# Optimization experiments

Hardware: AMD Instinct MI355X
Metric: run time of the kernel (lower is better)

Reference implementation:

```python
import jax, jax.numpy as jnp
import numpy as np

TEMPERATURE = 0.04


def _d3tod2(t):
    # 'c h w -> (h w) c'
    c, h, w = t.shape
    return jnp.transpose(t, (1, 2, 0)).reshape(h * w, c)


def setup_inputs() -> dict:
    key = jax.random.key(0)
    k1, k2 = jax.random.split(key)
    B, C, H, W = 4, 128, 96, 96
    # scale 0.05 keeps dot/temperature in a numerically sane range for exp
    x = jax.random.normal(k1, (B, C, H, W), dtype=jnp.float32) * 0.05
    label = jax.random.randint(k2, (B, 1, H, W), 0, 3, dtype=jnp.int32)
    return {"x": x, "label": label}


def reference(x, label):
    B, C, H, W = x.shape
    hw = H * W
    feat_1 = _d3tod2(x[0])                     # [HW, C]
    feat_2 = _d3tod2(x[1])                     # [HW, C]
    gt1 = label[0, 0].reshape(hw)              # [HW]
    gt2 = label[1, 0].reshape(hw)              # [HW]
    sim = jnp.exp(jnp.matmul(feat_1, feat_2.T) / TEMPERATURE)  # [HW, HW]
    mask = gt1[:, None] == gt2[None, :]        # [HW, HW] label-equality
    pos_sum = jnp.sum(jnp.where(mask, sim, jnp.zeros((), sim.dtype)))
    total_sum = jnp.sum(sim)
    loss = -jnp.log(pos_sum / total_sum) / (hw * hw)
    return loss
```

## Files before the change

### kernel.cpp

```cpp
#include <hip/hip_runtime.h>
#include <hip/hip_bf16.h>

#define HW 9216
#define CDIM 128
#define BM 256
#define BN 64
#define JT 4
#define GRID_I (HW / BM)
#define GRID_J (HW / (BN * JT))
#define NPART (GRID_I * GRID_J)
#define LDP (CDIM + 8)
#define SCH (HW / 512)

using bf16 = __hip_bfloat16;
typedef __attribute__((ext_vector_type(16))) float f32x16;
typedef __attribute__((ext_vector_type(8))) short s16x8;

#define EXP_SCALE 36.067376022224085f

#if __has_builtin(__builtin_amdgcn_exp2f)
#define FEXP2(x) __builtin_amdgcn_exp2f(x)
#else
#define FEXP2(x) exp2f(x)
#endif

__global__ __launch_bounds__(512) void sort_kernel(const int* __restrict__ label,
                                                   int* __restrict__ perm,
                                                   int* __restrict__ labs) {
    const int side = blockIdx.x;
    const int* L = label + side * HW;
    int* P = perm + side * HW;
    int* S = labs + side * HW;
    __shared__ int cnt[3][512];

    int t = threadIdx.x;
    int l[SCH];
    int c0 = 0, c1 = 0, c2 = 0;
#pragma unroll
    for (int k = 0; k < SCH; ++k) {
        l[k] = L[t * SCH + k];
        c0 += (l[k] == 0); c1 += (l[k] == 1); c2 += (l[k] == 2);
    }
    cnt[0][t] = c0; cnt[1][t] = c1; cnt[2][t] = c2;
    __syncthreads();

    for (int off = 1; off < 512; off <<= 1) {
        int v0 = cnt[0][t], v1 = cnt[1][t], v2 = cnt[2][t];
        int a0 = 0, a1 = 0, a2 = 0;
        if (t >= off) { a0 = cnt[0][t - off]; a1 = cnt[1][t - off]; a2 = cnt[2][t - off]; }
        __syncthreads();
        cnt[0][t] = v0 + a0; cnt[1][t] = v1 + a1; cnt[2][t] = v2 + a2;
        __syncthreads();
    }

    int i0 = cnt[0][t], i1 = cnt[1][t], i2 = cnt[2][t];
    int tl0 = cnt[0][511], tl1 = cnt[1][511];
    int o0 = i0 - c0;
    int o1 = tl0 + i1 - c1;
    int o2 = tl0 + tl1 + i2 - c2;
#pragma unroll
    for (int k = 0; k < SCH; ++k) {
        int lab = l[k];
        int pos = (lab == 0) ? o0++ : ((lab == 1) ? o1++ : o2++);
        P[pos] = t * SCH + k;
        S[pos] = lab;
    }
}

__global__ __launch_bounds__(256) void prep_kernel(const float* __restrict__ x,
                                                   const int* __restrict__ perm,
                                                   bf16* __restrict__ feat) {
    __shared__ float tile[64][65];
    const float* xs = x + (size_t)blockIdx.z * CDIM * HW;
    const int* permS = perm + blockIdx.z * HW;
    bf16* fs = feat + (size_t)blockIdx.z * HW * CDIM;
    float scale = (blockIdx.z == 0) ? EXP_SCALE : 1.0f;

    int p0 = blockIdx.x * 64;
    int c0 = blockIdx.y * 64;
    int t  = threadIdx.x;

    int pc = t & 63;
    int cr = t >> 6;
    int pidx = permS[p0 + pc];
#pragma unroll
    for (int i = 0; i < 16; ++i) {
        int cl = cr + i * 4;
        tile[cl][pc] = xs[(size_t)(c0 + cl) * HW + pidx];
    }
    __syncthreads();

    int cc = t & 63;
    int pr = t >> 6;
#pragma unroll
    for (int i = 0; i < 16; ++i) {
        int pl = pr + i * 4;
        fs[(size_t)(p0 + pl) * CDIM + c0 + cc] = __float2bfloat16(tile[cc][pl] * scale);
    }
}

__global__ __launch_bounds__(512, 4) void simsum_kernel(const bf16* __restrict__ feat1,
                                                        const bf16* __restrict__ feat2,
                                                        const int* __restrict__ labs,
                                                        float* __restrict__ partials) {
    __shared__ bf16 Bs[2][BN][LDP];
    __shared__ float red[16];

    const int* lab1s = labs;
    const int* lab2s = labs + HW;

    int t    = threadIdx.x;
    int w    = t >> 6;
    int lane = t & 63;
    int cl   = lane & 31;
    int hi   = lane >> 5;

    int i0  = blockIdx.x * BM;
    int jb  = blockIdx.y * (BN * JT);
    int r0w = i0 + w * 32;

    s16x8 af[8];
    {
        const bf16* arow = &feat1[(size_t)(r0w + cl) * CDIM + hi * 8];
#pragma unroll
        for (int s = 0; s < 8; ++s)
            af[s] = *(const s16x8*)(arow + s * 16);
    }

    int rlab  = lab1s[r0w];
    bool rowU = (rlab == lab1s[r0w + 31]);

    int4 g1i[4];
#pragma unroll
    for (int q = 0; q < 4; ++q)
        g1i[q] = *(const int4*)(&lab1s[r0w + 4 * hi + 8 * q]);

    int srow = t >> 4;
    int sch8 = (t & 15) * 8;
    s16x8 rb[2];

    auto load_tile = [&](int tt) {
        const bf16* base = &feat2[(size_t)(jb + tt * BN + srow) * CDIM + sch8];
        rb[0] = *(const s16x8*)(base);
        rb[1] = *(const s16x8*)(base + 32 * CDIM);
    };
    auto write_tile = [&](int b) {
        *(s16x8*)(&Bs[b][srow][sch8])      = rb[0];
        *(s16x8*)(&Bs[b][srow + 32][sch8]) = rb[1];
    };

    load_tile(0);  write_tile(0);
    load_tile(1);  write_tile(1);
    load_tile(2);
    asm volatile("s_waitcnt lgkmcnt(0)" ::: "memory");
    __builtin_amdgcn_sched_barrier(0);
    __builtin_amdgcn_s_barrier();

    float tot0 = 0.f, tot1 = 0.f, pos0 = 0.f, pos1 = 0.f;

#pragma unroll
    for (int tt = 0; tt < JT; ++tt) {
        int cb = jb + tt * BN;
        int laA = lab2s[cb];
        int laB = lab2s[cb + 32];
        bool uniA = rowU && (laA == lab2s[cb + 31]);
        bool uniB = rowU && (laB == lab2s[cb + 63]);
        int g2a = lab2s[cb + cl];
        int g2b = lab2s[cb + 32 + cl];

        f32x16 acc0 = {}, acc1 = {};
        __builtin_amdgcn_s_setprio(1);
#pragma unroll
        for (int s = 0; s < 8; ++s) {
            const bf16* bp = &Bs[tt & 1][cl][s * 16 + hi * 8];
            s16x8 b0 = *(const s16x8*)(bp);
            s16x8 b1 = *(const s16x8*)(bp + (size_t)32 * LDP);
            acc0 = __builtin_amdgcn_mfma_f32_32x32x16_bf16(af[s], b0, acc0, 0, 0, 0);
            acc1 = __builtin_amdgcn_mfma_f32_32x32x16_bf16(af[s], b1, acc1, 0, 0, 0);
        }
        __builtin_amdgcn_s_setprio(0);

        __builtin_amdgcn_sched_barrier(0);
        __builtin_amdgcn_s_barrier();

        if (tt + 2 < JT) write_tile(tt & 1);
        if (tt + 3 < JT) load_tile(tt + 3);

        {
            float a0 = 0.f, a1 = 0.f, a2 = 0.f, a3 = 0.f;
            float b0 = 0.f, b1 = 0.f, b2 = 0.f, b3 = 0.f;
#pragma unroll
            for (int r = 0; r < 4; ++r) {
                a0 += FEXP2(acc0[r]);
                a1 += FEXP2(acc0[r + 4]);
                a2 += FEXP2(acc0[r + 8]);
                a3 += FEXP2(acc0[r + 12]);
                b0 += FEXP2(acc1[r]);
                b1 += FEXP2(acc1[r + 4]);
                b2 += FEXP2(acc1[r + 8]);
                b3 += FEXP2(acc1[r + 12]);
            }
            float csA = (a0 + a1) + (a2 + a3);
            float csB = (b0 + b1) + (b2 + b3);
            tot0 += csA;
            tot1 += csB;
            if (uniA) {
                pos0 += (rlab == laA) ? csA : 0.f;
            } else {
#pragma unroll
                for (int r = 0; r < 16; ++r) {
                    int g1 = ((const int*)g1i)[r];
                    pos0 += (g1 == g2a) ? FEXP2(acc0[r]) : 0.f;
                }
            }
            if (uniB) {
                pos1 += (rlab == laB) ? csB : 0.f;
            } else {
#pragma unroll
                for (int r = 0; r < 16; ++r) {
                    int g1 = ((const int*)g1i)[r];
                    pos1 += (g1 == g2b) ? FEXP2(acc1[r]) : 0.f;
                }
            }
        }

        if (tt + 1 < JT) {
            asm volatile("s_waitcnt lgkmcnt(0)" ::: "memory");
            __builtin_amdgcn_sched_barrier(0);
            __builtin_amdgcn_s_barrier();
        }
    }

    float tot = tot0 + tot1, pos = pos0 + pos1;
#pragma unroll
    for (int off = 32; off; off >>= 1) {
        tot += __shfl_down(tot, off);
        pos += __shfl_down(pos, off);
    }
    if (lane == 0) { red[w * 2] = tot; red[w * 2 + 1] = pos; }
    __syncthreads();
    if (t == 0) {
        float T = 0.f, P = 0.f;
#pragma unroll
        for (int q = 0; q < 8; ++q) { T += red[q * 2]; P += red[q * 2 + 1]; }
        int bid = blockIdx.y * GRID_I + blockIdx.x;
        partials[bid * 2]     = T;
        partials[bid * 2 + 1] = P;
    }
}

__global__ __launch_bounds__(256) void finalize_kernel(const float* __restrict__ partials,
                                                       float* __restrict__ out) {
    double tot = 0.0, pos = 0.0;
    int t = threadIdx.x;
    for (int i = t; i < NPART; i += 256) {
        tot += (double)partials[i * 2];
        pos += (double)partials[i * 2 + 1];
    }
#pragma unroll
    for (int off = 32; off; off >>= 1) {
        tot += __shfl_down(tot, off);
        pos += __shfl_down(pos, off);
    }
    __shared__ double rt[4], rp[4];
    int w = t >> 6, lane = t & 63;
    if (lane == 0) { rt[w] = tot; rp[w] = pos; }
    __syncthreads();
    if (t == 0) {
        double T = rt[0] + rt[1] + rt[2] + rt[3];
        double P = rp[0] + rp[1] + rp[2] + rp[3];
        double hw2 = (double)HW * (double)HW;
        out[0] = (float)(-log(P / T) / hw2);
    }
}

extern "C" void kernel_launch(void* const* d_in, const int* in_sizes, int n_in,
                              void* d_out, int out_size, void* d_ws, size_t ws_size,
                              hipStream_t stream) {
    const float* x     = (const float*)d_in[0];
    const int*   label = (const int*)d_in[1];
    float*       out   = (float*)d_out;

    bf16* feat = (bf16*)d_ws;
    char* pp   = (char*)d_ws + 2 * (size_t)HW * CDIM * sizeof(bf16);
    int*  perm = (int*)pp;
    int*  labs = (int*)(pp + 2 * (size_t)HW * sizeof(int));
    float* parts = (float*)(pp + 4 * (size_t)HW * sizeof(int));

    sort_kernel<<<2, 512, 0, stream>>>(label, perm, labs);

    dim3 g1(HW / 64, CDIM / 64, 2);
    prep_kernel<<<g1, 256, 0, stream>>>(x, perm, feat);

    dim3 g2(GRID_I, GRID_J);
    simsum_kernel<<<g2, 512, 0, stream>>>(feat, feat + (size_t)HW * CDIM, labs, parts);

    finalize_kernel<<<1, 256, 0, stream>>>(parts, out);
}
```

Baseline: 58.40 us.

## Software-pipeline exp epilogue behind next tile's MFMAs and scatter via inverse permutation

The sort kernel now writes an inverse permutation, so the prep kernel reads x with coalesced contiguous loads and scatters whole bf16 rows to their sorted positions instead of gathering. In the similarity kernel, each tile's exp and sum epilogue is deferred by one iteration so it runs after the next tile's MFMAs are issued, which lets transcendental work overlap matrix work. The register-held row labels are dropped in favour of reloading them from global memory on the rare non-uniform path. Holding two extra accumulator sets raises register pressure and may hurt occupancy under the 512x4 launch bound.

New measurement: 58.63 us. No clear change (+0.4%).

```diff
diff --git a/kernel.cpp b/kernel.cpp
--- a/kernel.cpp
+++ b/kernel.cpp
@@ -25,12 +25,12 @@
 #endif
 
 __global__ __launch_bounds__(512) void sort_kernel(const int* __restrict__ label,
-                                                   int* __restrict__ perm,
+                                                   int* __restrict__ pinv,
                                                    int* __restrict__ labs) {
     const int side = blockIdx.x;
     const int* L = label + side * HW;
-    int* P = perm + side * HW;
-    int* S = labs + side * HW;
+    int* Pi = pinv + side * HW;
+    int* S  = labs + side * HW;
     __shared__ int cnt[3][512];
 
     int t = threadIdx.x;
@@ -62,17 +62,17 @@
     for (int k = 0; k < SCH; ++k) {
         int lab = l[k];
         int pos = (lab == 0) ? o0++ : ((lab == 1) ? o1++ : o2++);
-        P[pos] = t * SCH + k;
+        Pi[t * SCH + k] = pos;
         S[pos] = lab;
     }
 }
 
 __global__ __launch_bounds__(256) void prep_kernel(const float* __restrict__ x,
-                                                   const int* __restrict__ perm,
+                                                   const int* __restrict__ pinv,
                                                    bf16* __restrict__ feat) {
     __shared__ float tile[64][65];
     const float* xs = x + (size_t)blockIdx.z * CDIM * HW;
-    const int* permS = perm + blockIdx.z * HW;
+    const int* PiS = pinv + blockIdx.z * HW;
     bf16* fs = feat + (size_t)blockIdx.z * HW * CDIM;
     float scale = (blockIdx.z == 0) ? EXP_SCALE : 1.0f;
 
@@ -82,11 +82,10 @@
 
     int pc = t & 63;
     int cr = t >> 6;
-    int pidx = permS[p0 + pc];
 #pragma unroll
     for (int i = 0; i < 16; ++i) {
         int cl = cr + i * 4;
-        tile[cl][pc] = xs[(size_t)(c0 + cl) * HW + pidx];
+        tile[cl][pc] = xs[(size_t)(c0 + cl) * HW + p0 + pc];
     }
     __syncthreads();
 
@@ -95,7 +94,8 @@
 #pragma unroll
     for (int i = 0; i < 16; ++i) {
         int pl = pr + i * 4;
-        fs[(size_t)(p0 + pl) * CDIM + c0 + cc] = __float2bfloat16(tile[cc][pl] * scale);
+        int drow = PiS[p0 + pl];
+        fs[(size_t)drow * CDIM + c0 + cc] = __float2bfloat16(tile[cc][pl] * scale);
     }
 }
 
@@ -129,11 +129,6 @@
 
     int rlab  = lab1s[r0w];
     bool rowU = (rlab == lab1s[r0w + 31]);
-
-    int4 g1i[4];
-#pragma unroll
-    for (int q = 0; q < 4; ++q)
-        g1i[q] = *(const int4*)(&lab1s[r0w + 4 * hi + 8 * q]);
 
     int srow = t >> 4;
     int sch8 = (t & 15) * 8;
@@ -158,6 +153,50 @@
 
     float tot0 = 0.f, tot1 = 0.f, pos0 = 0.f, pos1 = 0.f;
 
+    f32x16 pA = {}, pB = {};
+    bool puA = true, puB = true;
+    int plA = 0, plB = 0, pg2a = 0, pg2b = 0;
+
+    auto epilogue = [&](const f32x16& accA, const f32x16& accB,
+                        bool uniA, bool uniB, int laA, int laB,
+                        int g2a, int g2b) {
+        float a0 = 0.f, a1 = 0.f, a2 = 0.f, a3 = 0.f;
+        float b0 = 0.f, b1 = 0.f, b2 = 0.f, b3 = 0.f;
+#pragma unroll
+        for (int r = 0; r < 4; ++r) {
+            a0 += FEXP2(accA[r]);
+            a1 += FEXP2(accA[r + 4]);
+            a2 += FEXP2(accA[r + 8]);
+            a3 += FEXP2(accA[r + 12]);
+            b0 += FEXP2(accB[r]);
+            b1 += FEXP2(accB[r + 4]);
+            b2 += FEXP2(accB[r + 8]);
+            b3 += FEXP2(accB[r + 12]);
+        }
+        float csA = (a0 + a1) + (a2 + a3);
+        float csB = (b0 + b1) + (b2 + b3);
+        tot0 += csA;
+        tot1 += csB;
+        if (__builtin_expect(uniA, 1)) {
+            pos0 += (rlab == laA) ? csA : 0.f;
+        } else {
+#pragma unroll
+            for (int r = 0; r < 16; ++r) {
+                int g1 = lab1s[r0w + (r & 3) + 8 * (r >> 2) + 4 * hi];
+                pos0 += (g1 == g2a) ? FEXP2(accA[r]) : 0.f;
+            }
+        }
+        if (__builtin_expect(uniB, 1)) {
+            pos1 += (rlab == laB) ? csB : 0.f;
+        } else {
+#pragma unroll
+            for (int r = 0; r < 16; ++r) {
+                int g1 = lab1s[r0w + (r & 3) + 8 * (r >> 2) + 4 * hi];
+                pos1 += (g1 == g2b) ? FEXP2(accB[r]) : 0.f;
+            }
+        }
+    };
+
 #pragma unroll
     for (int tt = 0; tt < JT; ++tt) {
         int cb = jb + tt * BN;
@@ -186,43 +225,9 @@
         if (tt + 2 < JT) write_tile(tt & 1);
         if (tt + 3 < JT) load_tile(tt + 3);
 
-        {
-            float a0 = 0.f, a1 = 0.f, a2 = 0.f, a3 = 0.f;
-            float b0 = 0.f, b1 = 0.f, b2 = 0.f, b3 = 0.f;
-#pragma unroll
-            for (int r = 0; r < 4; ++r) {
-                a0 += FEXP2(acc0[r]);
-                a1 += FEXP2(acc0[r + 4]);
-                a2 += FEXP2(acc0[r + 8]);
-                a3 += FEXP2(acc0[r + 12]);
-                b0 += FEXP2(acc1[r]);
-                b1 += FEXP2(acc1[r + 4]);
-                b2 += FEXP2(acc1[r + 8]);
-                b3 += FEXP2(acc1[r + 12]);
-            }
-            float csA = (a0 + a1) + (a2 + a3);
-            float csB = (b0 + b1) + (b2 + b3);
-            tot0 += csA;
-            tot1 += csB;
-            if (uniA) {
-                pos0 += (rlab == laA) ? csA : 0.f;
-            } else {
-#pragma unroll
-                for (int r = 0; r < 16; ++r) {
-                    int g1 = ((const int*)g1i)[r];
-                    pos0 += (g1 == g2a) ? FEXP2(acc0[r]) : 0.f;
-                }
-            }
-            if (uniB) {
-                pos1 += (rlab == laB) ? csB : 0.f;
-            } else {
-#pragma unroll
-                for (int r = 0; r < 16; ++r) {
-                    int g1 = ((const int*)g1i)[r];
-                    pos1 += (g1 == g2b) ? FEXP2(acc1[r]) : 0.f;
-                }
-            }
-        }
+        if (tt > 0) epilogue(pA, pB, puA, puB, plA, plB, pg2a, pg2b);
+        pA = acc0; pB = acc1; puA = uniA; puB = uniB;
+        plA = laA; plB = laB; pg2a = g2a; pg2b = g2b;
 
         if (tt + 1 < JT) {
             asm volatile("s_waitcnt lgkmcnt(0)" ::: "memory");
@@ -230,6 +235,7 @@
             __builtin_amdgcn_s_barrier();
         }
     }
+    epilogue(pA, pB, puA, puB, plA, plB, pg2a, pg2b);
 
     float tot = tot0 + tot1, pos = pos0 + pos1;
 #pragma unroll
@@ -283,14 +289,14 @@
 
     bf16* feat = (bf16*)d_ws;
     char* pp   = (char*)d_ws + 2 * (size_t)HW * CDIM * sizeof(bf16);
-    int*  perm = (int*)pp;
+    int*  pinv = (int*)pp;
     int*  labs = (int*)(pp + 2 * (size_t)HW * sizeof(int));
     float* parts = (float*)(pp + 4 * (size_t)HW * sizeof(int));
 
-    sort_kernel<<<2, 512, 0, stream>>>(label, perm, labs);
+    sort_kernel<<<2, 512, 0, stream>>>(label, pinv, labs);
 
     dim3 g1(HW / 64, CDIM / 64, 2);
-    prep_kernel<<<g1, 256, 0, stream>>>(x, perm, feat);
+    prep_kernel<<<g1, 256, 0, stream>>>(x, pinv, feat);
 
     dim3 g2(GRID_I, GRID_J);
     simsum_kernel<<<g2, 512, 0, stream>>>(feat, feat + (size_t)HW * CDIM, labs, parts);
```
